# Kernel optimization log

Measured on AMD Instinct MI355X. Metric: run time of the kernel, lower is better.

Reference implementation:

```python
import jax, jax.numpy as jnp
import numpy as np

HS = [192, 96, 48, 24, 12, 6]
WS = [384, 192, 96, 48, 24, 12]
C = 64    # feature channels per pyramid level
F = 64    # num_features (conv output channels)
CIN = 2 * C + 2  # current + warped + 2 flow channels = 130
N = 4


def dense_image_warp(image, flow):
    """tfa.image.dense_image_warp: warped[b,y,x] = bilinear(image[b, y - flow_y, x - flow_x]).
    Boundary handling matches tfa._interpolate_bilinear: floor indices clipped to
    [0, size-2], interpolation alphas clipped to [0, 1]."""
    n, h, w, _ = image.shape
    gy, gx = jnp.meshgrid(jnp.arange(h, dtype=flow.dtype),
                          jnp.arange(w, dtype=flow.dtype), indexing='ij')
    qy = gy[None] - flow[..., 0]          # [N,H,W] query rows
    qx = gx[None] - flow[..., 1]          # [N,H,W] query cols
    y0 = jnp.clip(jnp.floor(qy), 0, h - 2).astype(jnp.int32)
    x0 = jnp.clip(jnp.floor(qx), 0, w - 2).astype(jnp.int32)
    ay = jnp.clip(qy - y0.astype(flow.dtype), 0.0, 1.0)[..., None]
    ax = jnp.clip(qx - x0.astype(flow.dtype), 0.0, 1.0)[..., None]
    b = jnp.arange(n)[:, None, None]
    tl = image[b, y0, x0]
    tr = image[b, y0, x0 + 1]
    bl = image[b, y0 + 1, x0]
    br = image[b, y0 + 1, x0 + 1]
    top = tl + (tr - tl) * ax
    bot = bl + (br - bl) * ax
    return top + (bot - top) * ay


def separable_conv1x1(x, dw, pw, bias):
    # SeparableConv2D with 1x1 kernel: depthwise per-channel scale, then pointwise matmul.
    return jnp.einsum('nhwc,cf->nhwf', x * dw, pw) + bias


def _forward(xcs, xps, fls, dws, pws, bs):
    outs = []
    for i in range(6):
        # _warp: dense_image_warp(x_prev, -flow)
        warped = dense_image_warp(xps[i], -fls[i])
        x = jnp.concatenate([xcs[i], warped, fls[i]], axis=-1)  # [N,H,W,130]
        outs.append(separable_conv1x1(x, dws[i], pws[i], bs[i]))
    return tuple(outs)


def setup_inputs() -> dict:
    key = jax.random.key(0)
    d = {}
    for i in range(6):
        h, w = HS[i], WS[i]
        ks = jax.random.split(jax.random.fold_in(key, i), 6)
        d[f'xc{i}'] = jax.random.normal(ks[0], (N, h, w, C), jnp.float32)
        d[f'xp{i}'] = jax.random.normal(ks[1], (N, h, w, C), jnp.float32)
        d[f'fl{i}'] = jax.random.normal(ks[2], (N, h, w, 2), jnp.float32) * 2.0
        d[f'dw{i}'] = jax.random.normal(ks[3], (CIN,), jnp.float32) * 0.1
        d[f'pw{i}'] = jax.random.normal(ks[4], (CIN, F), jnp.float32) * 0.05
        d[f'bias{i}'] = jnp.zeros((F,), jnp.float32)
    return d


def reference(xc0, xc1, xc2, xc3, xc4, xc5,
              xp0, xp1, xp2, xp3, xp4, xp5,
              fl0, fl1, fl2, fl3, fl4, fl5,
              dw0, dw1, dw2, dw3, dw4, dw5,
              pw0, pw1, pw2, pw3, pw4, pw5,
              bias0, bias1, bias2, bias3, bias4, bias5):
    xcs = (xc0, xc1, xc2, xc3, xc4, xc5)
    xps = (xp0, xp1, xp2, xp3, xp4, xp5)
    fls = (fl0, fl1, fl2, fl3, fl4, fl5)
    dws = (dw0, dw1, dw2, dw3, dw4, dw5)
    pws = (pw0, pw1, pw2, pw3, pw4, pw5)
    bs = (bias0, bias1, bias2, bias3, bias4, bias5)
    return _forward(xcs, xps, fls, dws, pws, bs)
```

## Files before the change

kernel.cpp:

```cpp
#include <hip/hip_runtime.h>


typedef __attribute__((ext_vector_type(8))) short bf16x8;
typedef __attribute__((ext_vector_type(4))) float f32x4;

#define WS_LVL_STRIDE 17408

__device__ inline unsigned rne_bf16_bits(float f) {
  unsigned u = __builtin_bit_cast(unsigned, f);
  u += 0x7fffu + ((u >> 16) & 1u);
  return u >> 16;
}
__device__ inline int pack_bf16x2(float a, float b) {
  return (int)(rne_bf16_bits(a) | (rne_bf16_bits(b) << 16));
}

struct LevelArgs {
  const float* __restrict__ xc;
  const float* __restrict__ xp;
  const float* __restrict__ fl;
  float* __restrict__ out;
  const char* __restrict__ wsl;
  int H, W, npix, block_start;
};
struct KArgs { LevelArgs lv[6]; int total_blocks; };

struct PrepLevel {
  const float* __restrict__ dw;
  const float* __restrict__ pw;
  const float* __restrict__ bias;
  char* __restrict__ wsl;
};
struct PrepArgs { PrepLevel lv[6]; };

__global__ void prep_kernel(PrepArgs pa) {
  const PrepLevel P = pa.lv[blockIdx.x];
  int4* __restrict__ frag = (int4*)P.wsl;
  for (int e = (int)threadIdx.x; e < 1024; e += 256) {
    const int kt = e >> 8;
    const int nt = (e >> 6) & 3;
    const int lane = e & 63;
    const int n = nt * 16 + (lane & 15);
    const int kb = kt * 32 + ((lane >> 4) & 3) * 8;
    int v[4];
#pragma unroll
    for (int jj = 0; jj < 4; ++jj) {
      const int k0 = kb + jj * 2;
      const float w0 = P.dw[k0] * P.pw[(size_t)k0 * 64 + n];
      const float w1 = P.dw[k0 + 1] * P.pw[(size_t)(k0 + 1) * 64 + n];
      v[jj] = pack_bf16x2(w0, w1);
    }
    frag[e] = make_int4(v[0], v[1], v[2], v[3]);
  }
  float* __restrict__ tab = (float*)(P.wsl + 16384);
  if (threadIdx.x < 64) {
    const int f = (int)threadIdx.x;
    tab[f] = P.bias[f];
    tab[64 + f] = P.dw[128] * P.pw[128 * 64 + f];
    tab[128 + f] = P.dw[129] * P.pw[129 * 64 + f];
  }
}

#define SWZ(r, o) \
  ((((unsigned)(r)) << 7) | (((unsigned)(o)) ^ ((((unsigned)(r)) & 7u) << 4)))

__global__ __launch_bounds__(256, 5) void flowwarp_mfma(KArgs ka) {
  __shared__ __align__(16) char lds_raw[256 * 128];

  const int nb = ka.total_blocks;
  const int chunk = (nb + 7) >> 3;
  const int bp = (int)blockIdx.x;
  const int b = (bp & 7) * chunk + (bp >> 3);
  if (b >= nb) return;

  int Lr = 0;
#pragma unroll
  for (int i = 1; i < 6; ++i) Lr = (b >= ka.lv[i].block_start) ? i : Lr;
  const int L = __builtin_amdgcn_readfirstlane(Lr);
  const LevelArgs A = ka.lv[L];

  const int q = (int)threadIdx.x;
  const int p0 = (b - A.block_start) * 256;
  const int W = A.W, H = A.H;

  {
    int p = p0 + q;
    if (p > A.npix - 1) p = A.npix - 1;
    const int x = p % W;
    const int t = p / W;
    const int y = t % H;
    const int n = t / H;

    const float fl0 = A.fl[2 * (size_t)p];
    const float fl1 = A.fl[2 * (size_t)p + 1];

    const float qy = (float)y + fl0;
    const float qx = (float)x + fl1;
    const float fy = fminf(fmaxf(floorf(qy), 0.0f), (float)(H - 2));
    const float fx = fminf(fmaxf(floorf(qx), 0.0f), (float)(W - 2));
    const int y0 = (int)fy, x0 = (int)fx;
    const float ay = fminf(fmaxf(qy - fy, 0.0f), 1.0f);
    const float ax = fminf(fmaxf(qx - fx, 0.0f), 1.0f);

    const float* __restrict__ base =
        A.xp + ((size_t)((n * H + y0) * W + x0)) * 64;
    const int W64 = W * 64;
    const float4* __restrict__ tl4 = (const float4*)base;
    const float4* __restrict__ tr4 = (const float4*)(base + 64);
    const float4* __restrict__ bl4 = (const float4*)(base + W64);
    const float4* __restrict__ br4 = (const float4*)(base + W64 + 64);

#pragma unroll 1
    for (int bq = 0; bq < 4; ++bq) {
      float4 rtl[4], rtr[4], rbl[4], rbr[4];
#pragma unroll
      for (int i = 0; i < 4; ++i) {
        rtl[i] = tl4[bq * 4 + i];
        rtr[i] = tr4[bq * 4 + i];
        rbl[i] = bl4[bq * 4 + i];
        rbr[i] = br4[bq * 4 + i];
      }
      int v[8];
#pragma unroll
      for (int i = 0; i < 4; ++i) {
        const float atl[4] = {rtl[i].x, rtl[i].y, rtl[i].z, rtl[i].w};
        const float atr[4] = {rtr[i].x, rtr[i].y, rtr[i].z, rtr[i].w};
        const float abl[4] = {rbl[i].x, rbl[i].y, rbl[i].z, rbl[i].w};
        const float abr[4] = {rbr[i].x, rbr[i].y, rbr[i].z, rbr[i].w};
        float wv[4];
#pragma unroll
        for (int j = 0; j < 4; ++j) {
          const float top = fmaf(atr[j] - atl[j], ax, atl[j]);
          const float bot = fmaf(abr[j] - abl[j], ax, abl[j]);
          wv[j] = fmaf(bot - top, ay, top);
        }
        v[i * 2] = pack_bf16x2(wv[0], wv[1]);
        v[i * 2 + 1] = pack_bf16x2(wv[2], wv[3]);
      }
      *(int4*)(lds_raw + SWZ(q, bq * 32)) = make_int4(v[0], v[1], v[2], v[3]);
      *(int4*)(lds_raw + SWZ(q, bq * 32 + 16)) =
          make_int4(v[4], v[5], v[6], v[7]);
    }
  }
  __syncthreads();

  const int lane = q & 63;
  const int w = q >> 6;
  const int m16 = lane & 15;
  const int q4l = lane >> 4;

  const int4* __restrict__ bfr = (const int4*)A.wsl;
  bf16x8 Bf[4][4];
#pragma unroll
  for (int kt = 0; kt < 4; ++kt)
#pragma unroll
    for (int nt = 0; nt < 4; ++nt)
      Bf[kt][nt] = __builtin_bit_cast(bf16x8, bfr[(kt * 4 + nt) * 64 + lane]);

  const float* __restrict__ tab = (const float*)(A.wsl + 16384);
  float bv[4], t0v[4], t1v[4];
#pragma unroll
  for (int nt = 0; nt < 4; ++nt) {
    const int col = nt * 16 + m16;
    bv[nt] = tab[col];
    t0v[nt] = tab[64 + col];
    t1v[nt] = tab[128 + col];
  }
  const float2* __restrict__ flg = (const float2*)A.fl;

#pragma unroll 1
  for (int mt = 0; mt < 4; ++mt) {
    const int lrow = w * 64 + mt * 16;
    float2 fle[4];
#pragma unroll
    for (int i = 0; i < 4; ++i) {
      int pr = p0 + lrow + q4l * 4 + i;
      if (pr > A.npix - 1) pr = A.npix - 1;
      fle[i] = flg[pr];
    }
    int pm = p0 + lrow + m16;
    if (pm > A.npix - 1) pm = A.npix - 1;
    const float* __restrict__ xcp = A.xc + (size_t)pm * 64 + q4l * 8;
    const float4 a0 = *(const float4*)xcp;
    const float4 a1 = *(const float4*)(xcp + 4);
    const float4 a2 = *(const float4*)(xcp + 32);
    const float4 a3 = *(const float4*)(xcp + 36);
    int av[8];
    av[0] = pack_bf16x2(a0.x, a0.y); av[1] = pack_bf16x2(a0.z, a0.w);
    av[2] = pack_bf16x2(a1.x, a1.y); av[3] = pack_bf16x2(a1.z, a1.w);
    av[4] = pack_bf16x2(a2.x, a2.y); av[5] = pack_bf16x2(a2.z, a2.w);
    av[6] = pack_bf16x2(a3.x, a3.y); av[7] = pack_bf16x2(a3.z, a3.w);
    const bf16x8 A0 = __builtin_bit_cast(bf16x8, make_int4(av[0], av[1], av[2], av[3]));
    const bf16x8 A1 = __builtin_bit_cast(bf16x8, make_int4(av[4], av[5], av[6], av[7]));
    const int rr = lrow + m16;
    const bf16x8 A2 = __builtin_bit_cast(
        bf16x8, *(const int4*)(lds_raw + SWZ(rr, q4l * 16)));
    const bf16x8 A3 = __builtin_bit_cast(
        bf16x8, *(const int4*)(lds_raw + SWZ(rr, 64 + q4l * 16)));

    f32x4 acc[4] = {{0.f, 0.f, 0.f, 0.f}, {0.f, 0.f, 0.f, 0.f},
                    {0.f, 0.f, 0.f, 0.f}, {0.f, 0.f, 0.f, 0.f}};
#pragma unroll
    for (int nt = 0; nt < 4; ++nt) {
      acc[nt] = __builtin_amdgcn_mfma_f32_16x16x32_bf16(A0, Bf[0][nt], acc[nt], 0, 0, 0);
      acc[nt] = __builtin_amdgcn_mfma_f32_16x16x32_bf16(A1, Bf[1][nt], acc[nt], 0, 0, 0);
      acc[nt] = __builtin_amdgcn_mfma_f32_16x16x32_bf16(A2, Bf[2][nt], acc[nt], 0, 0, 0);
      acc[nt] = __builtin_amdgcn_mfma_f32_16x16x32_bf16(A3, Bf[3][nt], acc[nt], 0, 0, 0);
    }

#pragma unroll
    for (int i = 0; i < 4; ++i) {
      const int prow = p0 + lrow + q4l * 4 + i;
      if (prow < A.npix) {
        float* __restrict__ orow = A.out + (size_t)prow * 64 + m16;
#pragma unroll
        for (int nt = 0; nt < 4; ++nt)
          orow[nt * 16] = acc[nt][i] + bv[nt] + fle[i].x * t0v[nt] + fle[i].y * t1v[nt];
      }
    }
  }
}

extern "C" void kernel_launch(void* const* d_in, const int* in_sizes, int n_in,
                              void* d_out, int out_size, void* d_ws, size_t ws_size,
                              hipStream_t stream) {
  static const int HS[6] = {192, 96, 48, 24, 12, 6};
  static const int WS[6] = {384, 192, 96, 48, 24, 12};
  PrepArgs pa;
  KArgs ka;
  int bstart = 0;
  size_t ooff = 0;
  for (int i = 0; i < 6; ++i) {
    char* wsl = (char*)d_ws + (size_t)i * WS_LVL_STRIDE;
    pa.lv[i].dw   = (const float*)d_in[6 * i + 3];
    pa.lv[i].pw   = (const float*)d_in[6 * i + 4];
    pa.lv[i].bias = (const float*)d_in[6 * i + 5];
    pa.lv[i].wsl  = wsl;
    ka.lv[i].xc  = (const float*)d_in[6 * i + 0];
    ka.lv[i].xp  = (const float*)d_in[6 * i + 1];
    ka.lv[i].fl  = (const float*)d_in[6 * i + 2];
    ka.lv[i].out = (float*)d_out + ooff;
    ka.lv[i].wsl = wsl;
    const int npix = 4 * HS[i] * WS[i];
    ka.lv[i].H = HS[i];
    ka.lv[i].W = WS[i];
    ka.lv[i].npix = npix;
    ka.lv[i].block_start = bstart;
    bstart += (npix + 255) / 256;
    ooff += (size_t)npix * 64;
  }
  ka.total_blocks = bstart;
  prep_kernel<<<dim3(6), dim3(256), 0, stream>>>(pa);
  const int chunk = (bstart + 7) >> 3;
  flowwarp_mfma<<<dim3(chunk * 8), dim3(256), 0, stream>>>(ka);
}
```

Baseline: 415.4 us.

## Vectorize output stores via permuted weight columns, prefetch xc, drop block barrier

The pointwise weight fragments are permuted so each lane's four accumulator tiles hold four contiguous output channels. Each lane can then write one 16-byte nontemporal store per row instead of four strided scalar stores. The block-wide barrier becomes an LDS waitcnt, which is valid because each wave reads only the LDS rows it wrote itself. Flow values are fetched with lane shuffles instead of reloading them from global memory, and the next xc tile is prefetched with nontemporal loads. The risks are the extra registers the prefetch needs and an odd redundant term in the last output channel.

```diff
diff --git a/kernel.cpp b/kernel.cpp
--- a/kernel.cpp
+++ b/kernel.cpp
@@ -40,7 +40,7 @@
     const int kt = e >> 8;
     const int nt = (e >> 6) & 3;
     const int lane = e & 63;
-    const int n = nt * 16 + (lane & 15);
+    const int n = 4 * (lane & 15) + nt;
     const int kb = kt * 32 + ((lane >> 4) & 3) * 8;
     int v[4];
 #pragma unroll
@@ -82,6 +82,8 @@
   const int q = (int)threadIdx.x;
   const int p0 = (b - A.block_start) * 256;
   const int W = A.W, H = A.H;
+
+  float fl0, fl1;
 
   {
     int p = p0 + q;
@@ -91,8 +93,8 @@
     const int y = t % H;
     const int n = t / H;
 
-    const float fl0 = A.fl[2 * (size_t)p];
-    const float fl1 = A.fl[2 * (size_t)p + 1];
+    fl0 = A.fl[2 * (size_t)p];
+    fl1 = A.fl[2 * (size_t)p + 1];
 
     const float qy = (float)y + fl0;
     const float qx = (float)x + fl1;
@@ -105,14 +107,14 @@
     const float* __restrict__ base =
         A.xp + ((size_t)((n * H + y0) * W + x0)) * 64;
     const int W64 = W * 64;
-    const float4* __restrict__ tl4 = (const float4*)base;
-    const float4* __restrict__ tr4 = (const float4*)(base + 64);
-    const float4* __restrict__ bl4 = (const float4*)(base + W64);
-    const float4* __restrict__ br4 = (const float4*)(base + W64 + 64);
+    const f32x4* __restrict__ tl4 = (const f32x4*)base;
+    const f32x4* __restrict__ tr4 = (const f32x4*)(base + 64);
+    const f32x4* __restrict__ bl4 = (const f32x4*)(base + W64);
+    const f32x4* __restrict__ br4 = (const f32x4*)(base + W64 + 64);
 
 #pragma unroll 1
     for (int bq = 0; bq < 4; ++bq) {
-      float4 rtl[4], rtr[4], rbl[4], rbr[4];
+      f32x4 rtl[4], rtr[4], rbl[4], rbr[4];
 #pragma unroll
       for (int i = 0; i < 4; ++i) {
         rtl[i] = tl4[bq * 4 + i];
@@ -123,15 +125,11 @@
       int v[8];
 #pragma unroll
       for (int i = 0; i < 4; ++i) {
-        const float atl[4] = {rtl[i].x, rtl[i].y, rtl[i].z, rtl[i].w};
-        const float atr[4] = {rtr[i].x, rtr[i].y, rtr[i].z, rtr[i].w};
-        const float abl[4] = {rbl[i].x, rbl[i].y, rbl[i].z, rbl[i].w};
-        const float abr[4] = {rbr[i].x, rbr[i].y, rbr[i].z, rbr[i].w};
         float wv[4];
 #pragma unroll
         for (int j = 0; j < 4; ++j) {
-          const float top = fmaf(atr[j] - atl[j], ax, atl[j]);
-          const float bot = fmaf(abr[j] - abl[j], ax, abl[j]);
+          const float top = fmaf(rtr[i][j] - rtl[i][j], ax, rtl[i][j]);
+          const float bot = fmaf(rbr[i][j] - rbl[i][j], ax, rbl[i][j]);
           wv[j] = fmaf(bot - top, ay, top);
         }
         v[i * 2] = pack_bf16x2(wv[0], wv[1]);
@@ -142,7 +140,7 @@
           make_int4(v[4], v[5], v[6], v[7]);
     }
   }
-  __syncthreads();
+  asm volatile("s_waitcnt lgkmcnt(0)" ::: "memory");
 
   const int lane = q & 63;
   const int w = q >> 6;
@@ -158,38 +156,37 @@
       Bf[kt][nt] = __builtin_bit_cast(bf16x8, bfr[(kt * 4 + nt) * 64 + lane]);
 
   const float* __restrict__ tab = (const float*)(A.wsl + 16384);
-  float bv[4], t0v[4], t1v[4];
-#pragma unroll
-  for (int nt = 0; nt < 4; ++nt) {
-    const int col = nt * 16 + m16;
-    bv[nt] = tab[col];
-    t0v[nt] = tab[64 + col];
-    t1v[nt] = tab[128 + col];
-  }
-  const float2* __restrict__ flg = (const float2*)A.fl;
+  const f32x4 bvv  = *(const f32x4*)(tab + 4 * m16);
+  const f32x4 t0vv = *(const f32x4*)(tab + 64 + 4 * m16);
+  const f32x4 t1vv = *(const f32x4*)(tab + 128 + 4 * m16);
+
+  const int npix1 = A.npix - 1;
+  int pm = p0 + w * 64 + m16;
+  if (pm > npix1) pm = npix1;
+  const float* __restrict__ xcp = A.xc + (size_t)pm * 64 + q4l * 8;
+  f32x4 na0 = __builtin_nontemporal_load((const f32x4*)xcp);
+  f32x4 na1 = __builtin_nontemporal_load((const f32x4*)(xcp + 4));
+  f32x4 na2 = __builtin_nontemporal_load((const f32x4*)(xcp + 32));
+  f32x4 na3 = __builtin_nontemporal_load((const f32x4*)(xcp + 36));
 
 #pragma unroll 1
   for (int mt = 0; mt < 4; ++mt) {
     const int lrow = w * 64 + mt * 16;
-    float2 fle[4];
-#pragma unroll
-    for (int i = 0; i < 4; ++i) {
-      int pr = p0 + lrow + q4l * 4 + i;
-      if (pr > A.npix - 1) pr = A.npix - 1;
-      fle[i] = flg[pr];
-    }
-    int pm = p0 + lrow + m16;
-    if (pm > A.npix - 1) pm = A.npix - 1;
-    const float* __restrict__ xcp = A.xc + (size_t)pm * 64 + q4l * 8;
-    const float4 a0 = *(const float4*)xcp;
-    const float4 a1 = *(const float4*)(xcp + 4);
-    const float4 a2 = *(const float4*)(xcp + 32);
-    const float4 a3 = *(const float4*)(xcp + 36);
+    const f32x4 a0 = na0, a1 = na1, a2 = na2, a3 = na3;
+    if (mt < 3) {
+      int pn = p0 + lrow + 16 + m16;
+      if (pn > npix1) pn = npix1;
+      const float* __restrict__ xn = A.xc + (size_t)pn * 64 + q4l * 8;
+      na0 = __builtin_nontemporal_load((const f32x4*)xn);
+      na1 = __builtin_nontemporal_load((const f32x4*)(xn + 4));
+      na2 = __builtin_nontemporal_load((const f32x4*)(xn + 32));
+      na3 = __builtin_nontemporal_load((const f32x4*)(xn + 36));
+    }
     int av[8];
-    av[0] = pack_bf16x2(a0.x, a0.y); av[1] = pack_bf16x2(a0.z, a0.w);
-    av[2] = pack_bf16x2(a1.x, a1.y); av[3] = pack_bf16x2(a1.z, a1.w);
-    av[4] = pack_bf16x2(a2.x, a2.y); av[5] = pack_bf16x2(a2.z, a2.w);
-    av[6] = pack_bf16x2(a3.x, a3.y); av[7] = pack_bf16x2(a3.z, a3.w);
+    av[0] = pack_bf16x2(a0[0], a0[1]); av[1] = pack_bf16x2(a0[2], a0[3]);
+    av[2] = pack_bf16x2(a1[0], a1[1]); av[3] = pack_bf16x2(a1[2], a1[3]);
+    av[4] = pack_bf16x2(a2[0], a2[1]); av[5] = pack_bf16x2(a2[2], a2[3]);
+    av[6] = pack_bf16x2(a3[0], a3[1]); av[7] = pack_bf16x2(a3[2], a3[3]);
     const bf16x8 A0 = __builtin_bit_cast(bf16x8, make_int4(av[0], av[1], av[2], av[3]));
     const bf16x8 A1 = __builtin_bit_cast(bf16x8, make_int4(av[4], av[5], av[6], av[7]));
     const int rr = lrow + m16;
@@ -210,12 +207,19 @@
 
 #pragma unroll
     for (int i = 0; i < 4; ++i) {
+      const int srcl = mt * 16 + q4l * 4 + i;
+      const float f0i = __shfl(fl0, srcl);
+      const float f1i = __shfl(fl1, srcl);
       const int prow = p0 + lrow + q4l * 4 + i;
       if (prow < A.npix) {
-        float* __restrict__ orow = A.out + (size_t)prow * 64 + m16;
-#pragma unroll
-        for (int nt = 0; nt < 4; ++nt)
-          orow[nt * 16] = acc[nt][i] + bv[nt] + fle[i].x * t0v[nt] + fle[i].y * t1v[nt];
+        f32x4 o;
+        o[0] = acc[0][i] + bvv[0] + f0i * t0vv[0] + f1i * t1vv[0];
+        o[1] = acc[1][i] + bvv[1] + f0i * t0vv[1] + f1i * t1vv[1];
+        o[2] = acc[2][i] + bvv[2] + f0i * t0vv[2] + f1i * t1vv[2];
+        o[3] = acc[3][i] + bvv[3] + f0i * t1vv[3] * 0.0f + f1i * t1vv[3] +
+               f0i * t0vv[3];
+        __builtin_nontemporal_store(
+            o, (f32x4*)(A.out + (size_t)prow * 64 + 4 * m16));
       }
     }
   }
```

Result: slower. 426.1 us (+2.6%).
